# Kernel optimization log

Measured on AMD Instinct MI355X. Metric: run time of the kernel, lower is better.

The kernel has to match this reference:

```python
import jax, jax.numpy as jnp
import numpy as np

N = 100000      # nodes
E = 1600000     # edges (avg degree 16)
F_IN = 128      # input feature dim (lazy in_channels=-1)
HID = 256       # hidden_channels
OUT = 128       # out_channels
NCLS = 2        # final softmax classes


def _l2norm(x):
    # F.normalize(p=2, dim=-1) with eps clamp, as SAGEConv(normalize=True)
    n = jnp.linalg.norm(x, axis=-1, keepdims=True)
    return x / jnp.maximum(n, 1e-12)


def _sage(x, src, tgt, Wl, bl, Wr, n_nodes):
    # PyG SAGEConv: mean-aggregate source features at targets, then
    # out = lin_l(mean_aggr) + lin_r(x); lin_l has bias, lin_r does not.
    s = jax.ops.segment_sum(x[src], tgt, num_segments=n_nodes)          # [N, F]
    cnt = jax.ops.segment_sum(jnp.ones((src.shape[0],), x.dtype), tgt,
                              num_segments=n_nodes)                     # [N]
    mean = s / jnp.maximum(cnt, 1.0)[:, None]
    out = mean @ Wl.T + bl + x @ Wr.T
    return _l2norm(out)


def setup_inputs() -> dict:
    key = jax.random.key(0)
    ks = jax.random.split(key, 12)

    def glorot(k, o, i):
        lim = float(np.sqrt(6.0 / (o + i)))
        return jax.random.uniform(k, (o, i), jnp.float32, -lim, lim)

    return {
        "x": jax.random.normal(ks[0], (N, F_IN), jnp.float32),
        "edge_index": jax.random.randint(ks[1], (2, E), 0, N, dtype=jnp.int64),
        # conv1: SAGEConv(F_IN -> HID)
        "W1l": glorot(ks[2], HID, F_IN), "b1l": jnp.zeros((HID,), jnp.float32),
        "W1r": glorot(ks[3], HID, F_IN),
        # linear: HID -> OUT
        "Wlin": glorot(ks[4], OUT, HID), "blin": jnp.zeros((OUT,), jnp.float32),
        # conv2: SAGEConv(OUT -> OUT)
        "W2l": glorot(ks[5], OUT, OUT), "b2l": jnp.zeros((OUT,), jnp.float32),
        "W2r": glorot(ks[6], OUT, OUT),
        # linear2: OUT -> 2
        "Wlin2": glorot(ks[7], NCLS, OUT), "blin2": jnp.zeros((NCLS,), jnp.float32),
    }


def reference(x, edge_index, W1l, b1l, W1r, Wlin, blin, W2l, b2l, W2r, Wlin2, blin2):
    src, tgt = edge_index[0], edge_index[1]
    h = _sage(x, src, tgt, W1l, b1l, W1r, N)            # conv1, normalize
    h = jnp.maximum(h @ Wlin.T + blin, 0.0)             # linear + relu
    y = _sage(h, src, tgt, W2l, b2l, W2r, N)            # conv2, normalize
    logits = y @ Wlin2.T + blin2                        # linear2
    probs = jax.nn.softmax(logits, axis=1)
    return probs, y
```

## Files before the change

### kernel.cpp

```cpp
#include <hip/hip_runtime.h>
#include <hip/hip_bf16.h>
#include <hip/hip_fp8.h>

#define NN   100000
#define NE   1600000
#define NBK  196
#define BSH  9
#define EPB  8192
#define CAP  9216

typedef __attribute__((ext_vector_type(8))) short short8;
typedef __attribute__((ext_vector_type(4))) float f32x4;
typedef __attribute__((address_space(3))) uint  lds_uint;
typedef __attribute__((address_space(1))) const uint glb_uint;

__device__ __forceinline__ ushort f2bf(float f) {
    union { float f; uint u; } v; v.f = f;
    uint u = v.u;
    return (ushort)((u + 0x7FFFu + ((u >> 16) & 1u)) >> 16);
}
__device__ __forceinline__ float bf2f(uint b) {
    union { uint u; float f; } v; v.u = b << 16;
    return v.f;
}
__device__ __forceinline__ float fp8f(uint byte) {
    __hip_fp8_e4m3 t; t.__x = (__hip_fp8_storage_t)(byte & 0xffu);
    return (float)t;
}
__device__ __forceinline__ uint f2fp8(float f) {
    __hip_fp8_e4m3 t(f);
    return (uint)t.__x;
}
__device__ __forceinline__ int swz(int off) { return off ^ (((off >> 9) & 7) << 4); }

__device__ __forceinline__ void stageB(const ushort* __restrict__ W, char* Bs,
                                       int wave, int lane) {
#pragma unroll
    for (int k = 0; k < 8; ++k) {
        int base = k * 256 + wave * 64;
        __builtin_amdgcn_global_load_lds(
            (glb_uint*)(W + (size_t)(base + lane) * 8),
            (lds_uint*)(Bs + base * 16), 16, 0, 0);
    }
}

__global__ __launch_bounds__(256) void binit(int* __restrict__ bcursor) {
    int i = threadIdx.x;
    if (i < NBK) bcursor[i] = i * CAP;
}

__global__ __launch_bounds__(256) void bucket_scatter(const int* __restrict__ src,
                                                      const int* __restrict__ tgt,
                                                      int* __restrict__ bcursor,
                                                      uint* __restrict__ brec) {
    __shared__ int lh[NBK + 1];
    __shared__ int lcur[NBK];
    __shared__ int lbase[NBK];
    __shared__ uint lrec[EPB];
    __shared__ int ws[4];
    int tid = threadIdx.x;
    for (int i = tid; i < NBK; i += 256) lh[i] = 0;
    __syncthreads();
    int base4 = blockIdx.x * (EPB / 4);
#pragma unroll
    for (int k = 0; k < 8; ++k) {
        int i4 = base4 + k * 256 + tid;
        if (i4 < NE / 4) {
            int4 t = ((const int4*)tgt)[i4];
            atomicAdd(&lh[t.x >> BSH], 1);
            atomicAdd(&lh[t.y >> BSH], 1);
            atomicAdd(&lh[t.z >> BSH], 1);
            atomicAdd(&lh[t.w >> BSH], 1);
        }
    }
    __syncthreads();
    int v = (tid < NBK) ? lh[tid] : 0;
    int lane = tid & 63, wid = tid >> 6;
    int inc = v;
#pragma unroll
    for (int off = 1; off < 64; off <<= 1) {
        int u = __shfl_up(inc, off);
        if (lane >= off) inc += u;
    }
    if (lane == 63) ws[wid] = inc;
    __syncthreads();
    int woff = 0;
    for (int w = 0; w < wid; ++w) woff += ws[w];
    int ex = woff + inc - v;
    int nval = min(EPB, NE - blockIdx.x * EPB);
    if (tid < NBK) {
        lh[tid] = ex;
        lcur[tid] = ex;
        lbase[tid] = v ? atomicAdd(&bcursor[tid], v) : 0;
    }
    if (tid == 0) lh[NBK] = nval;
    __syncthreads();
#pragma unroll
    for (int k = 0; k < 8; ++k) {
        int i4 = base4 + k * 256 + tid;
        if (i4 < NE / 4) {
            int4 t = ((const int4*)tgt)[i4];
            int4 s = ((const int4*)src)[i4];
            int p;
            p = atomicAdd(&lcur[t.x >> BSH], 1); lrec[p] = ((uint)s.x << BSH) | (uint)(t.x & 511);
            p = atomicAdd(&lcur[t.y >> BSH], 1); lrec[p] = ((uint)s.y << BSH) | (uint)(t.y & 511);
            p = atomicAdd(&lcur[t.z >> BSH], 1); lrec[p] = ((uint)s.z << BSH) | (uint)(t.z & 511);
            p = atomicAdd(&lcur[t.w >> BSH], 1); lrec[p] = ((uint)s.w << BSH) | (uint)(t.w & 511);
        }
    }
    __syncthreads();
    for (int i = tid; i < nval; i += 256) {
        int lo = 0, hi = NBK;
        while (hi - lo > 1) { int mid = (lo + hi) >> 1; if (lh[mid] <= i) lo = mid; else hi = mid; }
        brec[lbase[lo] + (i - lh[lo])] = lrec[i];
    }
}

__global__ __launch_bounds__(256) void bucket_to_csr(const uint* __restrict__ brec,
                                                     const int* __restrict__ bcursor,
                                                     int* __restrict__ rowstart,
                                                     int* __restrict__ rowend,
                                                     int* __restrict__ sortedSrc) {
    __shared__ int cnt[512];
    __shared__ int cur[512];
    __shared__ int srt[CAP];
    __shared__ int ws[4];
    int b = blockIdx.x;
    int beg = b * CAP;
    int len = min(bcursor[b] - beg, CAP);
    int end = beg + len;
    int n0 = b << BSH;
    int ncnt = min(512, NN - n0);
    int tid = threadIdx.x;
    cnt[tid] = 0; cnt[tid + 256] = 0;
    __syncthreads();
    for (int i = beg + tid; i < end; i += 256)
        atomicAdd(&cnt[brec[i] & 511u], 1);
    __syncthreads();
    int c0 = cnt[2 * tid], c1 = cnt[2 * tid + 1];
    int s = c0 + c1;
    int lane = tid & 63, wid = tid >> 6;
    int inc = s;
#pragma unroll
    for (int off = 1; off < 64; off <<= 1) {
        int u = __shfl_up(inc, off);
        if (lane >= off) inc += u;
    }
    if (lane == 63) ws[wid] = inc;
    __syncthreads();
    int woff = 0;
    for (int w = 0; w < wid; ++w) woff += ws[w];
    int ex = woff + inc - s;
    cur[2 * tid] = ex; cur[2 * tid + 1] = ex + c0;
    if (2 * tid < ncnt) {
        rowstart[n0 + 2 * tid] = beg + ex;
        rowend[n0 + 2 * tid]   = beg + ex + c0;
    }
    if (2 * tid + 1 < ncnt) {
        rowstart[n0 + 2 * tid + 1] = beg + ex + c0;
        rowend[n0 + 2 * tid + 1]   = beg + ex + c0 + c1;
    }
    __syncthreads();
    for (int i = beg + tid; i < end; i += 256) {
        uint r = brec[i];
        int p = atomicAdd(&cur[r & 511u], 1);
        srt[p] = (int)(r >> BSH);
    }
    __syncthreads();
    for (int i = tid; i < len; i += 256)
        sortedSrc[beg + i] = srt[i];
}

__global__ __launch_bounds__(256) void gather_mean8(const uchar* __restrict__ t8,
                                                    const int* __restrict__ rowstart,
                                                    const int* __restrict__ rowend,
                                                    const int* __restrict__ sortedSrc,
                                                    ushort* __restrict__ mean) {
    int node = blockIdx.x * 4 + (threadIdx.x >> 6);
    if (node >= NN) return;
    int lane = threadIdx.x & 63;
    int q = lane >> 4, l = lane & 15;
    int beg = rowstart[node], end = rowend[node];
    float a0 = 0.f, a1 = 0.f, a2 = 0.f, a3 = 0.f;
    float a4 = 0.f, a5 = 0.f, a6 = 0.f, a7 = 0.f;
    float b0 = 0.f, b1 = 0.f, b2 = 0.f, b3 = 0.f;
    float b4 = 0.f, b5 = 0.f, b6 = 0.f, b7 = 0.f;
#define ACCA(v) { a0 += fp8f(v.x);       a1 += fp8f(v.x >> 8); \
                  a2 += fp8f(v.x >> 16); a3 += fp8f(v.x >> 24); \
                  a4 += fp8f(v.y);       a5 += fp8f(v.y >> 8); \
                  a6 += fp8f(v.y >> 16); a7 += fp8f(v.y >> 24); }
#define ACCB(v) { b0 += fp8f(v.x);       b1 += fp8f(v.x >> 8); \
                  b2 += fp8f(v.x >> 16); b3 += fp8f(v.x >> 24); \
                  b4 += fp8f(v.y);       b5 += fp8f(v.y >> 8); \
                  b6 += fp8f(v.y >> 16); b7 += fp8f(v.y >> 24); }
    int i = beg + q;
    for (; i + 4 < end; i += 8) {
        int s0 = sortedSrc[i];
        int s1 = sortedSrc[i + 4];
        uint2 v0 = *(const uint2*)&t8[(size_t)s0 * 128 + l * 8];
        uint2 v1 = *(const uint2*)&t8[(size_t)s1 * 128 + l * 8];
        ACCA(v0) ACCB(v1)
    }
    if (i < end) {
        int s0 = sortedSrc[i];
        uint2 v0 = *(const uint2*)&t8[(size_t)s0 * 128 + l * 8];
        ACCA(v0)
    }
#undef ACCA
#undef ACCB
    a0 += b0; a1 += b1; a2 += b2; a3 += b3;
    a4 += b4; a5 += b5; a6 += b6; a7 += b7;
#define CMB(a) a += __shfl_xor(a, 32); a += __shfl_xor(a, 16);
    CMB(a0) CMB(a1) CMB(a2) CMB(a3) CMB(a4) CMB(a5) CMB(a6) CMB(a7)
#undef CMB
    if (lane < 16) {
        float id = 1.0f / fmaxf((float)(end - beg), 1.0f);
        ushort p[8];
        p[0] = f2bf(a0 * id); p[1] = f2bf(a1 * id);
        p[2] = f2bf(a2 * id); p[3] = f2bf(a3 * id);
        p[4] = f2bf(a4 * id); p[5] = f2bf(a5 * id);
        p[6] = f2bf(a6 * id); p[7] = f2bf(a7 * id);
        *(uint4*)&mean[(size_t)node * 128 + l * 8] = *(uint4*)p;
    }
}

__global__ __launch_bounds__(256) void prep_w(const float* __restrict__ W1l,
                                              const float* __restrict__ W1r,
                                              const float* __restrict__ Wlin,
                                              const float* __restrict__ W2l,
                                              const float* __restrict__ W2r,
                                              ushort* __restrict__ Wcat1,
                                              ushort* __restrict__ Wlinb,
                                              ushort* __restrict__ Wcat2) {
    int i = blockIdx.x * 256 + threadIdx.x;
    if (i < 65536) {
        int e = i & 7, d = (i >> 3) & 63, g = (i >> 9) & 31, ch = i >> 14;
        int col = d & 15, kg = d >> 4, ks = g & 7, nt = g >> 3;
        int row = ch * 64 + nt * 16 + col;
        int k = ks * 32 + kg * 8 + e;
        float v = (k < 128) ? W1l[row * 128 + k] : W1r[row * 128 + k - 128];
        Wcat1[i] = f2bf(v);
    } else if (i < 98304) {
        int j = i - 65536;
        int e = j & 7, d = (j >> 3) & 63, g = (j >> 9) & 31, ch = j >> 14;
        int col = d & 15, kg = d >> 4, ks = g & 7, nt = g >> 3;
        int row = ch * 64 + nt * 16 + col;
        int k = ks * 32 + kg * 8 + e;
        Wlinb[j] = f2bf(Wlin[row * 256 + k]);
    } else {
        int j = i - 98304;
        int e = j & 7, d = (j >> 3) & 63, g = (j >> 9) & 31, ch = j >> 14;
        int col = d & 15, kg = d >> 4, ks = g & 7, nt = g >> 3;
        int row = ch * 64 + nt * 16 + col;
        int k = ks * 32 + kg * 8 + e;
        float v = (k < 128) ? W2l[row * 128 + k] : W2r[row * 128 + k - 128];
        Wcat2[j] = f2bf(v);
    }
}

__global__ __launch_bounds__(256) void xcvt(const float* __restrict__ x,
                                            ushort* __restrict__ xbf,
                                            uchar* __restrict__ x8) {
    int i = blockIdx.x * 256 + threadIdx.x;
    float4 v = ((const float4*)x)[i];
    ushort4 p;
    p.x = f2bf(v.x); p.y = f2bf(v.y); p.z = f2bf(v.z); p.w = f2bf(v.w);
    ((ushort4*)xbf)[i] = p;
    uint q = f2fp8(v.x) | (f2fp8(v.y) << 8) | (f2fp8(v.z) << 16) | (f2fp8(v.w) << 24);
    ((uint*)x8)[i] = q;
}

__global__ __launch_bounds__(256) void cvt8(const ushort* __restrict__ hr,
                                            uchar* __restrict__ hr8) {
    int i = blockIdx.x * 256 + threadIdx.x;
    uint4 v = ((const uint4*)hr)[i];
    uint lo = f2fp8(bf2f(v.x & 0xffffu)) | (f2fp8(bf2f(v.x >> 16)) << 8) |
              (f2fp8(bf2f(v.y & 0xffffu)) << 16) | (f2fp8(bf2f(v.y >> 16)) << 24);
    uint hi = f2fp8(bf2f(v.z & 0xffffu)) | (f2fp8(bf2f(v.z >> 16)) << 8) |
              (f2fp8(bf2f(v.w & 0xffffu)) << 16) | (f2fp8(bf2f(v.w >> 16)) << 24);
    uint2 o; o.x = lo; o.y = hi;
    ((uint2*)hr8)[i] = o;
}

__global__ __launch_bounds__(256) void conv1lin_mfma(const ushort* __restrict__ mean,
                                                     const ushort* __restrict__ xbf,
                                                     const ushort* __restrict__ Wcat,
                                                     const float* __restrict__ bias1,
                                                     const ushort* __restrict__ Wlin,
                                                     const float* __restrict__ blin,
                                                     ushort* __restrict__ hr) {
    __shared__ char As[64 * 512];
    __shared__ char Bs[64 * 512];
    int m0 = blockIdx.x * 64;
    int tid = threadIdx.x;
    int lane = tid & 63, wave = tid >> 6;
    stageB(Wcat, Bs, wave, lane);
    for (int c = tid; c < 2048; c += 256) {
        int m = c >> 5, kc = c & 31;
        int mm = min(m0 + m, NN - 1);
        uint4 v = (kc < 16) ? *(const uint4*)&mean[(size_t)mm * 128 + kc * 8]
                            : *(const uint4*)&xbf[(size_t)mm * 128 + (kc - 16) * 8];
        *(uint4*)(As + swz(m * 512 + kc * 16)) = v;
    }
    __syncthreads();

    int col = lane & 15, kg = lane >> 4;
    int mym = wave * 16 + col;
    short8 a[8];
#pragma unroll
    for (int ks = 0; ks < 8; ++ks)
        a[ks] = *(const short8*)(As + swz(mym * 512 + (ks * 32 + kg * 8) * 2));

    f32x4 acc[16];
    for (int ch = 0; ch < 4; ++ch) {
        if (ch) {
            __syncthreads();
            stageB(Wcat + (size_t)ch * 16384, Bs, wave, lane);
            __syncthreads();
        }
#pragma unroll
        for (int nt = 0; nt < 4; ++nt) {
            f32x4 c = {0.f, 0.f, 0.f, 0.f};
#pragma unroll
            for (int ks = 0; ks < 8; ++ks)
                c = __builtin_amdgcn_mfma_f32_16x16x32_bf16(
                    a[ks], *(const short8*)(Bs + ((nt * 8 + ks) * 64 + lane) * 16), c, 0, 0, 0);
            acc[ch * 4 + nt] = c;
        }
    }
    float ssq[4] = {0.f, 0.f, 0.f, 0.f};
#pragma unroll
    for (int i = 0; i < 16; ++i) {
        float b = bias1[i * 16 + col];
#pragma unroll
        for (int r = 0; r < 4; ++r) {
            acc[i][r] += b;
            ssq[r] += acc[i][r] * acc[i][r];
        }
    }
#pragma unroll
    for (int off = 1; off < 16; off <<= 1)
#pragma unroll
        for (int r = 0; r < 4; ++r) ssq[r] += __shfl_xor(ssq[r], off);
    float rn[4];
#pragma unroll
    for (int r = 0; r < 4; ++r) rn[r] = 1.0f / fmaxf(sqrtf(ssq[r]), 1e-12f);
#pragma unroll
    for (int i = 0; i < 16; ++i) {
        int chan = i * 16 + col;
#pragma unroll
        for (int r = 0; r < 4; ++r)
            *(ushort*)(As + swz((wave * 16 + kg * 4 + r) * 512 + chan * 2)) = f2bf(acc[i][r] * rn[r]);
    }
    short8 a2[8];
#pragma unroll
    for (int ks = 0; ks < 8; ++ks)
        a2[ks] = *(const short8*)(As + swz(mym * 512 + (ks * 32 + kg * 8) * 2));
    f32x4 acc2[8];
    for (int lc = 0; lc < 2; ++lc) {
        __syncthreads();
        stageB(Wlin + (size_t)lc * 16384, Bs, wave, lane);
        __syncthreads();
#pragma unroll
        for (int nt = 0; nt < 4; ++nt) {
            f32x4 c = {0.f, 0.f, 0.f, 0.f};
#pragma unroll
            for (int ks = 0; ks < 8; ++ks)
                c = __builtin_amdgcn_mfma_f32_16x16x32_bf16(
                    a2[ks], *(const short8*)(Bs + ((nt * 8 + ks) * 64 + lane) * 16), c, 0, 0, 0);
            acc2[lc * 4 + nt] = c;
        }
    }
#pragma unroll
    for (int i = 0; i < 8; ++i) {
        int chan = i * 16 + col;
        float b = blin[chan];
#pragma unroll
        for (int r = 0; r < 4; ++r) {
            int node = m0 + wave * 16 + kg * 4 + r;
            if (node < NN)
                hr[(size_t)node * 128 + chan] = f2bf(fmaxf(acc2[i][r] + b, 0.f));
        }
    }
}

__global__ __launch_bounds__(256) void conv2_mfma(const ushort* __restrict__ mean,
                                                  const ushort* __restrict__ hr,
                                                  const ushort* __restrict__ Wcat,
                                                  const float* __restrict__ bias,
                                                  const float* __restrict__ Wlin2,
                                                  const float* __restrict__ blin2,
                                                  float* __restrict__ probs,
                                                  float* __restrict__ yout) {
    __shared__ char As[64 * 512];
    __shared__ char Bs[64 * 512];
    int m0 = blockIdx.x * 64;
    int tid = threadIdx.x;
    int lane = tid & 63, wave = tid >> 6;
    stageB(Wcat, Bs, wave, lane);
    for (int c = tid; c < 2048; c += 256) {
        int m = c >> 5, kc = c & 31;
        int mm = min(m0 + m, NN - 1);
        uint4 v = (kc < 16) ? *(const uint4*)&mean[(size_t)mm * 128 + kc * 8]
                            : *(const uint4*)&hr[(size_t)mm * 128 + (kc - 16) * 8];
        *(uint4*)(As + swz(m * 512 + kc * 16)) = v;
    }
    __syncthreads();

    int col = lane & 15, kg = lane >> 4;
    int mym = wave * 16 + col;
    short8 a[8];
#pragma unroll
    for (int ks = 0; ks < 8; ++ks)
        a[ks] = *(const short8*)(As + swz(mym * 512 + (ks * 32 + kg * 8) * 2));

    f32x4 acc[8];
    for (int ch = 0; ch < 2; ++ch) {
        if (ch) {
            __syncthreads();
            stageB(Wcat + (size_t)ch * 16384, Bs, wave, lane);
            __syncthreads();
        }
#pragma unroll
        for (int nt = 0; nt < 4; ++nt) {
            f32x4 c = {0.f, 0.f, 0.f, 0.f};
#pragma unroll
            for (int ks = 0; ks < 8; ++ks)
                c = __builtin_amdgcn_mfma_f32_16x16x32_bf16(
                    a[ks], *(const short8*)(Bs + ((nt * 8 + ks) * 64 + lane) * 16), c, 0, 0, 0);
            acc[ch * 4 + nt] = c;
        }
    }
    float ssq[4] = {0.f, 0.f, 0.f, 0.f};
#pragma unroll
    for (int i = 0; i < 8; ++i) {
        float b = bias[i * 16 + col];
#pragma unroll
        for (int r = 0; r < 4; ++r) {
            acc[i][r] += b;
            ssq[r] += acc[i][r] * acc[i][r];
        }
    }
#pragma unroll
    for (int off = 1; off < 16; off <<= 1)
#pragma unroll
        for (int r = 0; r < 4; ++r) ssq[r] += __shfl_xor(ssq[r], off);
    float rn[4], p0[4] = {0.f,0.f,0.f,0.f}, p1[4] = {0.f,0.f,0.f,0.f};
#pragma unroll
    for (int r = 0; r < 4; ++r) rn[r] = 1.0f / fmaxf(sqrtf(ssq[r]), 1e-12f);
#pragma unroll
    for (int i = 0; i < 8; ++i) {
        int chan = i * 16 + col;
        float w0 = Wlin2[chan], w1 = Wlin2[128 + chan];
#pragma unroll
        for (int r = 0; r < 4; ++r) {
            float yv = acc[i][r] * rn[r];
            acc[i][r] = yv;
            p0[r] += yv * w0;
            p1[r] += yv * w1;
        }
    }
#pragma unroll
    for (int off = 1; off < 16; off <<= 1)
#pragma unroll
        for (int r = 0; r < 4; ++r) { p0[r] += __shfl_xor(p0[r], off); p1[r] += __shfl_xor(p1[r], off); }
#pragma unroll
    for (int r = 0; r < 4; ++r) {
        int node = m0 + wave * 16 + kg * 4 + r;
        if (node < NN) {
#pragma unroll
            for (int i = 0; i < 8; ++i)
                yout[(size_t)node * 128 + i * 16 + col] = acc[i][r];
            if (col == 0) {
                float l0 = p0[r] + blin2[0], l1 = p1[r] + blin2[1];
                float mx = fmaxf(l0, l1);
                float e0 = expf(l0 - mx), e1 = expf(l1 - mx);
                float inv = 1.0f / (e0 + e1);
                probs[(size_t)node * 2 + 0] = e0 * inv;
                probs[(size_t)node * 2 + 1] = e1 * inv;
            }
        }
    }
}

extern "C" void kernel_launch(void* const* d_in, const int* in_sizes, int n_in,
                              void* d_out, int out_size, void* d_ws, size_t ws_size,
                              hipStream_t stream) {
    const float* x     = (const float*)d_in[0];
    const int*   ei    = (const int*)d_in[1];
    const int*   src   = ei;
    const int*   tgt   = ei + NE;
    const float* W1l   = (const float*)d_in[2];
    const float* b1l   = (const float*)d_in[3];
    const float* W1r   = (const float*)d_in[4];
    const float* Wlin  = (const float*)d_in[5];
    const float* blin  = (const float*)d_in[6];
    const float* W2l   = (const float*)d_in[7];
    const float* b2l   = (const float*)d_in[8];
    const float* W2r   = (const float*)d_in[9];
    const float* Wlin2 = (const float*)d_in[10];
    const float* blin2 = (const float*)d_in[11];

    float* probs = (float*)d_out;
    float* y     = (float*)d_out + 2 * NN;

    int*    bcursor   = (int*)d_ws;
    int*    rowstart  = bcursor + NBK;
    int*    rowend    = rowstart + NN;
    uint*   brec      = (uint*)(rowend + NN);
    int*    sortedSrc = (int*)(brec + (size_t)NBK * CAP);
    ushort* Wcat1     = (ushort*)(sortedSrc + (size_t)NBK * CAP);
    ushort* Wlinb     = Wcat1 + 65536;
    ushort* Wcat2     = Wlinb + 32768;
    ushort* xbf       = Wcat2 + 32768;
    ushort* hr        = xbf + (size_t)NN * 128;
    ushort* mean      = hr + (size_t)NN * 128;
    uchar*  x8        = (uchar*)(mean + (size_t)NN * 128);
    uchar*  hr8       = x8 + (size_t)NN * 128;

    const int NEB = (NE + EPB - 1) / EPB;

    prep_w<<<512, 256, 0, stream>>>(W1l, W1r, Wlin, W2l, W2r, Wcat1, Wlinb, Wcat2);
    xcvt<<<NN * 32 / 256, 256, 0, stream>>>(x, xbf, x8);

    binit<<<1, 256, 0, stream>>>(bcursor);
    bucket_scatter<<<NEB, 256, 0, stream>>>(src, tgt, bcursor, brec);
    bucket_to_csr<<<NBK, 256, 0, stream>>>(brec, bcursor, rowstart, rowend, sortedSrc);

    gather_mean8<<<(NN + 3) / 4, 256, 0, stream>>>(x8, rowstart, rowend, sortedSrc, mean);
    conv1lin_mfma<<<(NN + 63) / 64, 256, 0, stream>>>(mean, xbf, Wcat1, b1l,
                                                      Wlinb, blin, hr);
    cvt8<<<NN * 128 / 8 / 256, 256, 0, stream>>>(hr, hr8);
    gather_mean8<<<(NN + 3) / 4, 256, 0, stream>>>(hr8, rowstart, rowend, sortedSrc, mean);
    conv2_mfma<<<(NN + 63) / 64, 256, 0, stream>>>(mean, hr, Wcat2, b2l,
                                                   Wlin2, blin2, probs, y);
}
```

Baseline: 283.0 us.

## Load MFMA A-operands directly from global, unroll gather, fold bucket init

Both MFMA kernels now load their A fragments straight from global memory into registers and no longer stage them through a swizzled LDS tile. This drops the LDS round trip, and conv2 loses its As buffer entirely, which lowers LDS use and may raise occupancy. The fp8 gather-mean loop is unrolled to four in-flight edge loads per iteration for more memory-level parallelism. The separate binit launch is folded into prep_w to save one kernel launch. Direct global A loads are less coalesced, since each lane reads 16 bytes from a different row.

Measured after the change: 276.4 us. -2.3%, faster.

```diff
diff --git a/kernel.cpp b/kernel.cpp
--- a/kernel.cpp
+++ b/kernel.cpp
@@ -42,11 +42,6 @@
             (glb_uint*)(W + (size_t)(base + lane) * 8),
             (lds_uint*)(Bs + base * 16), 16, 0, 0);
     }
-}
-
-__global__ __launch_bounds__(256) void binit(int* __restrict__ bcursor) {
-    int i = threadIdx.x;
-    if (i < NBK) bcursor[i] = i * CAP;
 }
 
 __global__ __launch_bounds__(256) void bucket_scatter(const int* __restrict__ src,
@@ -194,14 +189,18 @@
                   b4 += fp8f(v.y);       b5 += fp8f(v.y >> 8); \
                   b6 += fp8f(v.y >> 16); b7 += fp8f(v.y >> 24); }
     int i = beg + q;
-    for (; i + 4 < end; i += 8) {
+    for (; i + 12 < end; i += 16) {
         int s0 = sortedSrc[i];
         int s1 = sortedSrc[i + 4];
+        int s2 = sortedSrc[i + 8];
+        int s3 = sortedSrc[i + 12];
         uint2 v0 = *(const uint2*)&t8[(size_t)s0 * 128 + l * 8];
         uint2 v1 = *(const uint2*)&t8[(size_t)s1 * 128 + l * 8];
-        ACCA(v0) ACCB(v1)
-    }
-    if (i < end) {
+        uint2 v2 = *(const uint2*)&t8[(size_t)s2 * 128 + l * 8];
+        uint2 v3 = *(const uint2*)&t8[(size_t)s3 * 128 + l * 8];
+        ACCA(v0) ACCB(v1) ACCA(v2) ACCB(v3)
+    }
+    for (; i < end; i += 4) {
         int s0 = sortedSrc[i];
         uint2 v0 = *(const uint2*)&t8[(size_t)s0 * 128 + l * 8];
         ACCA(v0)
@@ -231,7 +230,9 @@
                                               const float* __restrict__ W2r,
                                               ushort* __restrict__ Wcat1,
                                               ushort* __restrict__ Wlinb,
-                                              ushort* __restrict__ Wcat2) {
+                                              ushort* __restrict__ Wcat2,
+                                              int* __restrict__ bcursor) {
+    if (blockIdx.x == 0 && threadIdx.x < NBK) bcursor[threadIdx.x] = (int)threadIdx.x * CAP;
     int i = blockIdx.x * 256 + threadIdx.x;
     if (i < 65536) {
         int e = i & 7, d = (i >> 3) & 63, g = (i >> 9) & 31, ch = i >> 14;
@@ -294,22 +295,18 @@
     int m0 = blockIdx.x * 64;
     int tid = threadIdx.x;
     int lane = tid & 63, wave = tid >> 6;
-    stageB(Wcat, Bs, wave, lane);
-    for (int c = tid; c < 2048; c += 256) {
-        int m = c >> 5, kc = c & 31;
-        int mm = min(m0 + m, NN - 1);
-        uint4 v = (kc < 16) ? *(const uint4*)&mean[(size_t)mm * 128 + kc * 8]
-                            : *(const uint4*)&xbf[(size_t)mm * 128 + (kc - 16) * 8];
-        *(uint4*)(As + swz(m * 512 + kc * 16)) = v;
-    }
-    __syncthreads();
-
     int col = lane & 15, kg = lane >> 4;
     int mym = wave * 16 + col;
+    int mm = min(m0 + mym, NN - 1);
+    stageB(Wcat, Bs, wave, lane);
     short8 a[8];
 #pragma unroll
-    for (int ks = 0; ks < 8; ++ks)
-        a[ks] = *(const short8*)(As + swz(mym * 512 + (ks * 32 + kg * 8) * 2));
+    for (int ks = 0; ks < 4; ++ks)
+        a[ks] = *(const short8*)&mean[(size_t)mm * 128 + ks * 32 + kg * 8];
+#pragma unroll
+    for (int ks = 4; ks < 8; ++ks)
+        a[ks] = *(const short8*)&xbf[(size_t)mm * 128 + (ks - 4) * 32 + kg * 8];
+    __syncthreads();
 
     f32x4 acc[16];
     for (int ch = 0; ch < 4; ++ch) {
@@ -392,27 +389,22 @@
                                                   const float* __restrict__ blin2,
                                                   float* __restrict__ probs,
                                                   float* __restrict__ yout) {
-    __shared__ char As[64 * 512];
     __shared__ char Bs[64 * 512];
     int m0 = blockIdx.x * 64;
     int tid = threadIdx.x;
     int lane = tid & 63, wave = tid >> 6;
-    stageB(Wcat, Bs, wave, lane);
-    for (int c = tid; c < 2048; c += 256) {
-        int m = c >> 5, kc = c & 31;
-        int mm = min(m0 + m, NN - 1);
-        uint4 v = (kc < 16) ? *(const uint4*)&mean[(size_t)mm * 128 + kc * 8]
-                            : *(const uint4*)&hr[(size_t)mm * 128 + (kc - 16) * 8];
-        *(uint4*)(As + swz(m * 512 + kc * 16)) = v;
-    }
-    __syncthreads();
-
     int col = lane & 15, kg = lane >> 4;
     int mym = wave * 16 + col;
+    int mm = min(m0 + mym, NN - 1);
+    stageB(Wcat, Bs, wave, lane);
     short8 a[8];
 #pragma unroll
-    for (int ks = 0; ks < 8; ++ks)
-        a[ks] = *(const short8*)(As + swz(mym * 512 + (ks * 32 + kg * 8) * 2));
+    for (int ks = 0; ks < 4; ++ks)
+        a[ks] = *(const short8*)&mean[(size_t)mm * 128 + ks * 32 + kg * 8];
+#pragma unroll
+    for (int ks = 4; ks < 8; ++ks)
+        a[ks] = *(const short8*)&hr[(size_t)mm * 128 + (ks - 4) * 32 + kg * 8];
+    __syncthreads();
 
     f32x4 acc[8];
     for (int ch = 0; ch < 2; ++ch) {
@@ -520,10 +512,10 @@
 
     const int NEB = (NE + EPB - 1) / EPB;
 
-    prep_w<<<512, 256, 0, stream>>>(W1l, W1r, Wlin, W2l, W2r, Wcat1, Wlinb, Wcat2);
+    prep_w<<<512, 256, 0, stream>>>(W1l, W1r, Wlin, W2l, W2r, Wcat1, Wlinb, Wcat2,
+                                    bcursor);
     xcvt<<<NN * 32 / 256, 256, 0, stream>>>(x, xbf, x8);
 
-    binit<<<1, 256, 0, stream>>>(bcursor);
     bucket_scatter<<<NEB, 256, 0, stream>>>(src, tgt, bcursor, brec);
     bucket_to_csr<<<NBK, 256, 0, stream>>>(brec, bcursor, rowstart, rowend, sortedSrc);
 
```
